# Kernel optimization log

Measured on AMD Instinct MI355X. Metric: run time of the kernel, lower is better.

The kernel has to match this reference:

```python
import jax, jax.numpy as jnp
import numpy as np

B, L, D, T, NL = 64, 512, 512, 5000, 2


def setup_inputs() -> dict:
    key = jax.random.key(0)
    k1, k2, k3, k4 = jax.random.split(key, 4)
    enc_output = jax.random.normal(k1, (B, L, D), dtype=jnp.float32)
    # stands in for the row/col-normalized tag co-occurrence matrix (values in [0, 0.01])
    ui_adj = jax.random.uniform(k2, (T, T), dtype=jnp.float32) * 0.01
    # one GCN weight matrix per layer in the layer_stack
    Ws = jax.random.normal(k3, (NL, D, D), dtype=jnp.float32) / np.sqrt(D).astype(np.float32)
    # event ids are 1-indexed in the original (it indexes with e - 1)
    event_type = jax.random.randint(k4, (B, L), 1, T + 1, dtype=jnp.int64)
    slf_attn_mask = jnp.zeros((B, L, L), dtype=bool)
    non_pad_mask = jnp.ones((B, L), dtype=bool)
    return {"enc_output": enc_output, "ui_adj": ui_adj, "Ws": Ws,
            "event_type": event_type, "slf_attn_mask": slf_attn_mask,
            "non_pad_mask": non_pad_mask}


def reference(enc_output, ui_adj, Ws, event_type, slf_attn_mask, non_pad_mask):
    # --- batched per-sample adjacency gather (replaces the Python loop) ---
    idx = event_type - 1                                   # [B, L] 0-indexed
    sub = ui_adj[idx[:, :, None], idx[:, None, :]]         # [B, L, L] = ui_adj[e-1,:][:, e-1]
    diag = ui_adj[idx, idx]                                # [B, L]   = ui_adj[e-1, e-1]
    adj = sub + diag[:, None, :]                           # vector broadcasts across rows, as in torch
    # --- GNN layer stack (hGCN layer ~ relu(A @ X @ W)) ---
    x = enc_output
    for l in range(Ws.shape[0]):                           # small fixed n_layers loop
        x = jax.nn.relu(jnp.einsum('bij,bjd->bid', adj, x) @ Ws[l])
    # --- mean pool over sequence ---
    return x.mean(axis=1)                                  # [B, D]
```

## Files before the change

kernel.cpp:

```cpp
#include <hip/hip_runtime.h>

typedef unsigned short u16;
typedef unsigned int u32;
typedef __bf16 bf16x8 __attribute__((ext_vector_type(8)));
typedef float f32x16 __attribute__((ext_vector_type(16)));
typedef int i32x4 __attribute__((ext_vector_type(4)));
typedef u32 u32x2 __attribute__((ext_vector_type(2)));
typedef u32 u32x4 __attribute__((ext_vector_type(4)));

#define T_ 5000
#define CAP 96

__device__ __forceinline__ u16 f2bf(float f) {
  u32 u = __float_as_uint(f);
  u += 0x7fffu + ((u >> 16) & 1u);
  return (u16)(u >> 16);
}
__device__ __forceinline__ float bf2f(u32 bits16) {
  return __uint_as_float(bits16 << 16);
}

__device__ __forceinline__ void gload_lds16(const u16* g, u16* l) {
  __builtin_amdgcn_global_load_lds(
      (__attribute__((address_space(1))) void*)(u16*)g,
      (__attribute__((address_space(3))) void*)l, 16, 0, 0);
}

__device__ __forceinline__ u32 lds_off(const void* p) {
  return (u32)(uintptr_t)(__attribute__((address_space(3))) const void*)p;
}

__device__ __forceinline__ u32 swz(int row, int kb) {
  return (u32)((row >> 1) * 128 +
               ((((row & 1) << 6) | kb) ^ (((row >> 1) & 7) << 4)));
}

__global__ void prep_k(const float* __restrict__ src, u16* __restrict__ dst,
                       int* __restrict__ cnt) {
  __shared__ float tile[32][33];
  const int tx = threadIdx.x, ty = threadIdx.y;
  const int a0 = blockIdx.x * 32;
  const int b0 = blockIdx.y * 32;
  const size_t zoff = (size_t)blockIdx.z * (512 * 512);
  const float* s = src + zoff;
  u16* d = dst + zoff;
#pragma unroll
  for (int r = 0; r < 4; ++r)
    tile[ty + r * 8][tx] = s[(size_t)(a0 + ty + r * 8) * 512 + b0 + tx];
  const int gid = ((blockIdx.z * 16 + blockIdx.y) * 16 + blockIdx.x) * 256 + ty * 32 + tx;
  if (gid < 5008) cnt[gid] = 0;
  __syncthreads();
#pragma unroll
  for (int r = 0; r < 4; ++r)
    d[(size_t)(b0 + ty + r * 8) * 512 + a0 + tx] = f2bf(tile[tx][ty + r * 8]);
}

__global__ void fill_k(const int* __restrict__ ev, const float* __restrict__ ui,
                       int2* __restrict__ cd, int* __restrict__ cnt,
                       int* __restrict__ list, int* __restrict__ ovf) {
  const int t = blockIdx.x * 256 + threadIdx.x;
  const int r = ev[t] - 1;
  int2 v;
  v.x = r;
  v.y = __float_as_int(ui[(size_t)r * (T_ + 1)]);
  cd[t] = v;
  const int pos = atomicAdd(&cnt[r], 1);
  if (pos < CAP) list[r * CAP + pos] = t;
  else { const int o = atomicAdd(&cnt[5000], 1); ovf[o] = t; }
}

__global__ __launch_bounds__(256)
void grow_gather(const float* __restrict__ ui, const int2* __restrict__ cd,
                 const int* __restrict__ cnt, const int* __restrict__ list,
                 const int* __restrict__ ovf, u16* __restrict__ adj) {
  __shared__ float row[5000];
  __shared__ int lst[CAP];
  const int r = blockIdx.x;
  int c = cnt[r];
  if (c > CAP) c = CAP;
  const int j = threadIdx.x * 2;
  if (c > 0) {
    const float* __restrict__ src = ui + (size_t)r * T_;
    for (int t = threadIdx.x; t < 1250; t += 256)
      *(float4*)&row[t * 4] = *(const float4*)&src[t * 4];
    if (threadIdx.x < c) lst[threadIdx.x] = list[r * CAP + threadIdx.x];
    __syncthreads();
    int q = 0;
    for (; q + 4 <= c; q += 4) {
      const int t0 = lst[q], t1 = lst[q + 1], t2 = lst[q + 2], t3 = lst[q + 3];
      const int4 p0 = *(const int4*)&cd[((t0 >> 9) << 9) + j];
      const int4 p1 = *(const int4*)&cd[((t1 >> 9) << 9) + j];
      const int4 p2 = *(const int4*)&cd[((t2 >> 9) << 9) + j];
      const int4 p3 = *(const int4*)&cd[((t3 >> 9) << 9) + j];
      const u32 k0 = (u32)f2bf(row[p0.x] + __int_as_float(p0.y)) |
                     ((u32)f2bf(row[p0.z] + __int_as_float(p0.w)) << 16);
      const u32 k1 = (u32)f2bf(row[p1.x] + __int_as_float(p1.y)) |
                     ((u32)f2bf(row[p1.z] + __int_as_float(p1.w)) << 16);
      const u32 k2 = (u32)f2bf(row[p2.x] + __int_as_float(p2.y)) |
                     ((u32)f2bf(row[p2.z] + __int_as_float(p2.w)) << 16);
      const u32 k3 = (u32)f2bf(row[p3.x] + __int_as_float(p3.y)) |
                     ((u32)f2bf(row[p3.z] + __int_as_float(p3.w)) << 16);
      *(u32*)&adj[(size_t)t0 * 512 + j] = k0;
      *(u32*)&adj[(size_t)t1 * 512 + j] = k1;
      *(u32*)&adj[(size_t)t2 * 512 + j] = k2;
      *(u32*)&adj[(size_t)t3 * 512 + j] = k3;
    }
    for (; q < c; ++q) {
      const int t0 = lst[q];
      const int4 p0 = *(const int4*)&cd[((t0 >> 9) << 9) + j];
      const u32 k0 = (u32)f2bf(row[p0.x] + __int_as_float(p0.y)) |
                     ((u32)f2bf(row[p0.z] + __int_as_float(p0.w)) << 16);
      *(u32*)&adj[(size_t)t0 * 512 + j] = k0;
    }
  }
  if (r < 8) {
    const int n = cnt[5000];
    for (int q = r; q < n; q += 8) {
      const int t = ovf[q];
      const long rr = (long)cd[t].x;
      const float* __restrict__ rp = ui + rr * (long)T_;
      const int4 p = *(const int4*)&cd[((t >> 9) << 9) + j];
      const u32 pk = (u32)f2bf(rp[p.x] + __int_as_float(p.y)) |
                     ((u32)f2bf(rp[p.z] + __int_as_float(p.w)) << 16);
      *(u32*)&adj[(size_t)t * 512 + j] = pk;
    }
  }
}

template <int MODE, int BSRC>
__global__ __launch_bounds__(512, 2)
void gemm256(const u16* __restrict__ A, const void* __restrict__ Bv,
             u16* __restrict__ C, size_t strideA, size_t strideB, size_t strideC,
             float* __restrict__ P) {
  extern __shared__ u16 smem[];
  const int tid = threadIdx.x;
  const int lane = tid & 63;
  const int w = tid >> 6;
  const int wm = w >> 2, wn = w & 3;
  const int chunk = gridDim.x >> 3;
  const int wg = blockIdx.x;
  const int mapped = (wg & 7) * chunk + (wg >> 3);
  const int batch = mapped >> 2;
  const int tm = (mapped >> 1) & 1, tn = mapped & 1;
  const int m0 = tm << 8, n0 = tn << 8;
  const u16* __restrict__ Ab = A + (size_t)batch * strideA;

  const u16* gA[2];
  u32 ldA[2];
#pragma unroll
  for (int r = 0; r < 2; ++r) {
    const int c = r * 512 + tid;
    const int L = c * 16;
    const int pp = L >> 7;
    const int off = (L & 127) ^ ((pp & 7) << 4);
    const int m = pp * 2 + (off >> 6);
    const int kb = off & 63;
    gA[r] = Ab + (size_t)(m0 + m) * 512 + (kb >> 1);
    ldA[r] = (u32)((r * 512 + w * 64) * 8);
  }

  const u16* gB[2] = {nullptr, nullptr};
  u32 ldB[2] = {0, 0};
  if (BSRC == 0) {
    const u16* __restrict__ Bb = (const u16*)Bv + (size_t)batch * strideB;
#pragma unroll
    for (int r = 0; r < 2; ++r) {
      const int c = r * 512 + tid;
      const int L = c * 16;
      const int pp = L >> 7;
      const int off = (L & 127) ^ ((pp & 7) << 4);
      const int m = pp * 2 + (off >> 6);
      const int kb = off & 63;
      gB[r] = Bb + (size_t)(n0 + m) * 512 + (kb >> 1);
      ldB[r] = (u32)(32768 + (r * 512 + w * 64) * 8);
    }
  }

  const int dp = tid & 127;
  const int lq = tid >> 7;
  unsigned long long encB = 0;
  u32 boff0 = 0;
  u32x2 bs0[8], bs1[8];
  if (BSRC == 1) {
    encB = (unsigned long long)(uintptr_t)((const float*)Bv + (size_t)batch * strideB);
    boff0 = (u32)(((lq * 8) * 512 + n0 + dp * 2) * 4);
  }

#define BLOAD(t, S)                                                          \
  {                                                                          \
    const u32 ob = boff0 + (u32)(t) * 65536u;                                \
    _Pragma("unroll") for (int i = 0; i < 8; ++i)                            \
        asm volatile("global_load_dwordx2 %0, %1, %2"                        \
                     : "=v"(S[i])                                            \
                     : "v"(ob + (u32)i * 2048u), "s"(encB));                 \
  }

#define CONVERT_B(S)                                                         \
  {                                                                          \
    u32 wrd0[4], wrd1[4];                                                    \
    _Pragma("unroll") for (int jj = 0; jj < 4; ++jj) {                       \
      asm("v_cvt_pk_bf16_f32 %0, %1, %2"                                     \
          : "=v"(wrd0[jj]) : "v"(S[2 * jj].x), "v"(S[2 * jj + 1].x));        \
      asm("v_cvt_pk_bf16_f32 %0, %1, %2"                                     \
          : "=v"(wrd1[jj]) : "v"(S[2 * jj].y), "v"(S[2 * jj + 1].y));        \
    }                                                                        \
    const u32 by0 = (u32)dp * 128u + ((((u32)lq * 16u)) ^ (((u32)dp & 7u) << 4)); \
    const u32 by1 = (u32)dp * 128u + ((64u | ((u32)lq * 16u)) ^ (((u32)dp & 7u) << 4)); \
    u32x4 v0, v1;                                                            \
    v0.x = wrd0[0]; v0.y = wrd0[1]; v0.z = wrd0[2]; v0.w = wrd0[3];          \
    v1.x = wrd1[0]; v1.y = wrd1[1]; v1.z = wrd1[2]; v1.w = wrd1[3];          \
    *(u32x4*)((char*)smem + 65536 + by0) = v0;                               \
    *(u32x4*)((char*)smem + 65536 + by1) = v1;                               \
  }

  const int col = lane & 31;
  const int h16 = (lane >> 5) * 16;
  u32 aOff[4][2], bOff[2][2];
#pragma unroll
  for (int mf = 0; mf < 4; ++mf)
#pragma unroll
    for (int kk = 0; kk < 2; ++kk)
      aOff[mf][kk] = swz(wm * 128 + mf * 32 + col, kk * 32 + h16);
#pragma unroll
  for (int nf = 0; nf < 2; ++nf)
#pragma unroll
    for (int kk = 0; kk < 2; ++kk)
      bOff[nf][kk] = 65536u + swz(wn * 64 + nf * 32 + col, kk * 32 + h16);
  const u32 ldsBase = lds_off(smem);

  f32x16 acc[4][2] = {};

  auto stageA = [&](int t) {
    const u32 bo = (u32)(t & 3) * 8192;
#pragma unroll
    for (int r = 0; r < 2; ++r) gload_lds16(gA[r] + t * 32, smem + bo + ldA[r]);
  };
  auto stageB0 = [&](int t) {
    const u32 bo = (u32)(t & 3) * 8192;
#pragma unroll
    for (int r = 0; r < 2; ++r) gload_lds16(gB[r] + t * 32, smem + bo + ldB[r]);
  };

  if (BSRC == 0) {
    stageA(0); stageB0(0); stageA(1); stageB0(1); stageA(2); stageB0(2);
  } else {
    stageA(0); stageA(1); stageA(2);
    BLOAD(0, bs0); BLOAD(1, bs1);
  }

#pragma unroll
  for (int t = 0; t < 16; ++t) {
    if (BSRC == 0) {
      if (t <= 13)      asm volatile("s_waitcnt vmcnt(8)" ::: "memory");
      else if (t == 14) asm volatile("s_waitcnt vmcnt(4)" ::: "memory");
      else              asm volatile("s_waitcnt vmcnt(0)" ::: "memory");
      __builtin_amdgcn_sched_barrier(0);
      if (t + 3 < 16) { stageA(t + 3); stageB0(t + 3); }
      asm volatile("" ::: "memory");
      __builtin_amdgcn_s_barrier();
      asm volatile("" ::: "memory");
    } else {
      if (t == 0)              asm volatile("s_waitcnt vmcnt(8)" ::: "memory");
      else if (t <= 13)        asm volatile("s_waitcnt vmcnt(10)" ::: "memory");
      else if (t == 14)        asm volatile("s_waitcnt vmcnt(8)" ::: "memory");
      else                     asm volatile("s_waitcnt vmcnt(0)" ::: "memory");
      __builtin_amdgcn_sched_barrier(0);
      if (t & 1) { CONVERT_B(bs1); } else { CONVERT_B(bs0); }
      if (t + 3 < 16) stageA(t + 3);
      if (t + 2 < 16) { if (t & 1) { BLOAD(t + 2, bs1); } else { BLOAD(t + 2, bs0); } }
      asm volatile("s_waitcnt lgkmcnt(0)" ::: "memory");
      __builtin_amdgcn_s_barrier();
      asm volatile("" ::: "memory");
    }

    const u32 abase = ldsBase + (u32)(t & 3) * 16384;
    const u32 bbase = (BSRC == 0) ? abase : ldsBase;
    i32x4 braw[2][2], araw[4][2];
#pragma unroll
    for (int nf = 0; nf < 2; ++nf)
#pragma unroll
      for (int kk = 0; kk < 2; ++kk)
        asm volatile("ds_read_b128 %0, %1" : "=v"(braw[nf][kk]) : "v"(bbase + bOff[nf][kk]));
#pragma unroll
    for (int mf = 0; mf < 2; ++mf)
#pragma unroll
      for (int kk = 0; kk < 2; ++kk)
        asm volatile("ds_read_b128 %0, %1" : "=v"(araw[mf][kk]) : "v"(abase + aOff[mf][kk]));
#pragma unroll
    for (int mf = 2; mf < 4; ++mf)
#pragma unroll
      for (int kk = 0; kk < 2; ++kk)
        asm volatile("ds_read_b128 %0, %1" : "=v"(araw[mf][kk]) : "v"(abase + aOff[mf][kk]));

    asm volatile("s_waitcnt lgkmcnt(4)" ::: "memory");
    __builtin_amdgcn_sched_barrier(0);
    __builtin_amdgcn_s_setprio(1);
#pragma unroll
    for (int kk = 0; kk < 2; ++kk)
#pragma unroll
      for (int mf = 0; mf < 2; ++mf)
#pragma unroll
        for (int nf = 0; nf < 2; ++nf)
          acc[mf][nf] = __builtin_amdgcn_mfma_f32_32x32x16_bf16(
              __builtin_bit_cast(bf16x8, araw[mf][kk]),
              __builtin_bit_cast(bf16x8, braw[nf][kk]), acc[mf][nf], 0, 0, 0);
    asm volatile("s_waitcnt lgkmcnt(0)" ::: "memory");
    __builtin_amdgcn_sched_barrier(0);
#pragma unroll
    for (int kk = 0; kk < 2; ++kk)
#pragma unroll
      for (int mf = 2; mf < 4; ++mf)
#pragma unroll
        for (int nf = 0; nf < 2; ++nf)
          acc[mf][nf] = __builtin_amdgcn_mfma_f32_32x32x16_bf16(
              __builtin_bit_cast(bf16x8, araw[mf][kk]),
              __builtin_bit_cast(bf16x8, braw[nf][kk]), acc[mf][nf], 0, 0, 0);
    __builtin_amdgcn_s_setprio(0);
    asm volatile("" ::: "memory");
    __builtin_amdgcn_s_barrier();
    __builtin_amdgcn_sched_barrier(0);
  }
#undef BLOAD
#undef CONVERT_B

  u16* Cb = C + (size_t)batch * strideC;
  if (MODE == 0) {
#pragma unroll
    for (int mf = 0; mf < 4; ++mf) {
      const int rbase = m0 + wm * 128 + mf * 32 + 4 * (lane >> 5);
#pragma unroll
      for (int nf = 0; nf < 2; ++nf) {
        const int cc = n0 + wn * 64 + nf * 32 + col;
        const f32x16 v = acc[mf][nf];
#pragma unroll
        for (int g = 0; g < 4; ++g)
#pragma unroll
          for (int j = 0; j < 4; ++j)
            Cb[(size_t)(rbase + 8 * g + j) * 512 + cc] = f2bf(v[g * 4 + j]);
      }
    }
  } else if (MODE == 1) {
#pragma unroll
    for (int mf = 0; mf < 4; ++mf) {
      const int ibase = m0 + wm * 128 + mf * 32 + 4 * (lane >> 5);
#pragma unroll
      for (int nf = 0; nf < 2; ++nf) {
        const int d = n0 + wn * 64 + nf * 32 + col;
        const f32x16 v = acc[mf][nf];
#pragma unroll
        for (int g = 0; g < 4; ++g) {
          const int i = ibase + 8 * g;
          uint2 p;
          p.x = (u32)f2bf(fmaxf(v[g * 4 + 0], 0.f)) |
                ((u32)f2bf(fmaxf(v[g * 4 + 1], 0.f)) << 16);
          p.y = (u32)f2bf(fmaxf(v[g * 4 + 2], 0.f)) |
                ((u32)f2bf(fmaxf(v[g * 4 + 3], 0.f)) << 16);
          *(uint2*)&Cb[(size_t)d * 512 + i] = p;
        }
      }
    }
  } else {
    const int slot = tm * 2 + wm;
#pragma unroll
    for (int nf = 0; nf < 2; ++nf) {
      float s = 0.f;
#pragma unroll
      for (int mf = 0; mf < 4; ++mf) {
        const f32x16 v = acc[mf][nf];
#pragma unroll
        for (int r = 0; r < 16; ++r) s += fmaxf(v[r], 0.f);
      }
      s += __shfl_xor(s, 32);
      if (lane < 32) {
        const int d = n0 + wn * 64 + nf * 32 + lane;
        P[((size_t)batch * 4 + slot) * 512 + d] = s;
      }
    }
  }
}

__global__ void reduce_mean(const float* __restrict__ P, float* __restrict__ out) {
  const int t = blockIdx.x * 256 + threadIdx.x;
  const int b = t >> 9, d = t & 511;
  float s = 0.f;
#pragma unroll
  for (int q = 0; q < 4; ++q) s += P[((size_t)b * 4 + q) * 512 + d];
  out[t] = s * (1.0f / 512.0f);
}

extern "C" void kernel_launch(void* const* d_in, const int* in_sizes, int n_in,
                              void* d_out, int out_size, void* d_ws, size_t ws_size,
                              hipStream_t stream) {
  const float* enc = (const float*)d_in[0];
  const float* ui  = (const float*)d_in[1];
  const float* Ws  = (const float*)d_in[2];
  const int*   ev  = (const int*)d_in[3];
  float* out = (float*)d_out;

  char* ws = (char*)d_ws;
  const size_t SLAB = (size_t)64 * 512 * 512 * 2;
  u16* adj  = (u16*)(ws);
  u16* tbuf = (u16*)(ws + SLAB);
  u16* xb   = (u16*)(ws + 2 * SLAB);
  char* p = ws + 3 * SLAB;
  u16* wst  = (u16*)p;  p += (size_t)2 * 512 * 512 * 2;
  int2* cd  = (int2*)p; p += (size_t)32768 * 8;
  int* cnt  = (int*)p;  p += 5008 * 4;
  int* list = (int*)p;  p += (size_t)5000 * CAP * 4;
  int* ovf  = (int*)p;  p += (size_t)32768 * 4;
  float* P  = (float*)p;

  const size_t PS = (size_t)512 * 512;
  const size_t SMEM0 = 131072;
  const size_t SMEM1 = 81920;
  (void)hipFuncSetAttribute(reinterpret_cast<const void*>(gemm256<0, 1>),
                            hipFuncAttributeMaxDynamicSharedMemorySize, (int)SMEM1);
  (void)hipFuncSetAttribute(reinterpret_cast<const void*>(gemm256<1, 0>),
                            hipFuncAttributeMaxDynamicSharedMemorySize, (int)SMEM0);
  (void)hipFuncSetAttribute(reinterpret_cast<const void*>(gemm256<0, 0>),
                            hipFuncAttributeMaxDynamicSharedMemorySize, (int)SMEM0);
  (void)hipFuncSetAttribute(reinterpret_cast<const void*>(gemm256<2, 0>),
                            hipFuncAttributeMaxDynamicSharedMemorySize, (int)SMEM0);

  prep_k<<<dim3(16, 16, 2), dim3(32, 8), 0, stream>>>(Ws, wst, cnt);
  fill_k<<<128, 256, 0, stream>>>(ev, ui, cd, cnt, list, ovf);
  grow_gather<<<5000, 256, 0, stream>>>(ui, cd, cnt, list, ovf, adj);
  gemm256<0, 1><<<256, 512, SMEM1, stream>>>(adj, enc, tbuf, PS, PS, PS, nullptr);
  gemm256<1, 0><<<256, 512, SMEM0, stream>>>(tbuf, wst, xb, PS, 0, PS, nullptr);
  gemm256<0, 0><<<256, 512, SMEM0, stream>>>(adj, xb, tbuf, PS, PS, PS, nullptr);
  gemm256<2, 0><<<256, 512, SMEM0, stream>>>(tbuf, wst + PS, nullptr, PS, 0, 0, P);
  reduce_mean<<<128, 256, 0, stream>>>(P, out);
}
```

Before: 144.9 us.

## Split GEMMs into 256x128 tiles with triple-buffered LDS and higher occupancy

```diff
diff --git a/kernel.cpp b/kernel.cpp
--- a/kernel.cpp
+++ b/kernel.cpp
@@ -6,7 +6,6 @@
 typedef float f32x16 __attribute__((ext_vector_type(16)));
 typedef int i32x4 __attribute__((ext_vector_type(4)));
 typedef u32 u32x2 __attribute__((ext_vector_type(2)));
-typedef u32 u32x4 __attribute__((ext_vector_type(4)));
 
 #define T_ 5000
 #define CAP 96
@@ -15,9 +14,6 @@
   u32 u = __float_as_uint(f);
   u += 0x7fffu + ((u >> 16) & 1u);
   return (u16)(u >> 16);
-}
-__device__ __forceinline__ float bf2f(u32 bits16) {
-  return __uint_as_float(bits16 << 16);
 }
 
 __device__ __forceinline__ void gload_lds16(const u16* g, u16* l) {
@@ -127,66 +123,62 @@
   }
 }
 
-template <int MODE, int BSRC>
-__global__ __launch_bounds__(512, 2)
-void gemm256(const u16* __restrict__ A, const void* __restrict__ Bv,
-             u16* __restrict__ C, size_t strideA, size_t strideB, size_t strideC,
-             float* __restrict__ P) {
+template <int LAYER>
+__global__ __launch_bounds__(512, LAYER == 0 ? 2 : 4)
+void gemmT(const u16* __restrict__ adj, const void* __restrict__ Xv,
+           u16* __restrict__ tb) {
   extern __shared__ u16 smem[];
   const int tid = threadIdx.x;
   const int lane = tid & 63;
   const int w = tid >> 6;
-  const int wm = w >> 2, wn = w & 3;
-  const int chunk = gridDim.x >> 3;
+  const int wm = w >> 1;
+  const int wn = w & 1;
   const int wg = blockIdx.x;
-  const int mapped = (wg & 7) * chunk + (wg >> 3);
-  const int batch = mapped >> 2;
-  const int tm = (mapped >> 1) & 1, tn = mapped & 1;
-  const int m0 = tm << 8, n0 = tn << 8;
-  const u16* __restrict__ Ab = A + (size_t)batch * strideA;
-
-  const u16* gA[2];
-  u32 ldA[2];
-#pragma unroll
-  for (int r = 0; r < 2; ++r) {
-    const int c = r * 512 + tid;
-    const int L = c * 16;
-    const int pp = L >> 7;
-    const int off = (L & 127) ^ ((pp & 7) << 4);
-    const int m = pp * 2 + (off >> 6);
+  const int mapped = (wg & 7) * 64 + (wg >> 3);
+  const int batch = mapped >> 3;
+  const int sub = mapped & 7;
+  const int m0 = (sub >> 2) << 8;
+  const int n0i = (sub & 3) << 7;
+  const size_t PS = (size_t)512 * 512;
+  const u16* __restrict__ adjB = adj + batch * PS;
+
+  const u16* gAdj;
+  u32 ldAdj;
+  {
+    const int L = tid * 16;
+    const int p = L >> 7;
+    const int off = (L & 127) ^ ((p & 7) << 4);
+    const int mr = p * 2 + (off >> 6);
     const int kb = off & 63;
-    gA[r] = Ab + (size_t)(m0 + m) * 512 + (kb >> 1);
-    ldA[r] = (u32)((r * 512 + w * 64) * 8);
-  }
-
-  const u16* gB[2] = {nullptr, nullptr};
-  u32 ldB[2] = {0, 0};
-  if (BSRC == 0) {
-    const u16* __restrict__ Bb = (const u16*)Bv + (size_t)batch * strideB;
+    gAdj = adjB + (size_t)(n0i + mr) * 512 + (kb >> 1);
+    ldAdj = (u32)(w * 512);
+  }
+  const u16* gX[2] = {nullptr, nullptr};
+  u32 ldX[2] = {0, 0};
+  unsigned long long encB = 0;
+  u32 boff0 = 0;
+  const int dp = tid & 127;
+  const int lq = tid >> 7;
+  u32x2 bs0[8], bs1[8];
+  if (LAYER == 1) {
+    const u16* __restrict__ xbB = (const u16*)Xv + batch * PS;
 #pragma unroll
     for (int r = 0; r < 2; ++r) {
       const int c = r * 512 + tid;
       const int L = c * 16;
-      const int pp = L >> 7;
-      const int off = (L & 127) ^ ((pp & 7) << 4);
-      const int m = pp * 2 + (off >> 6);
+      const int p = L >> 7;
+      const int off = (L & 127) ^ ((p & 7) << 4);
+      const int mr = p * 2 + (off >> 6);
       const int kb = off & 63;
-      gB[r] = Bb + (size_t)(n0 + m) * 512 + (kb >> 1);
-      ldB[r] = (u32)(32768 + (r * 512 + w * 64) * 8);
-    }
-  }
-
-  const int dp = tid & 127;
-  const int lq = tid >> 7;
-  unsigned long long encB = 0;
-  u32 boff0 = 0;
-  u32x2 bs0[8], bs1[8];
-  if (BSRC == 1) {
-    encB = (unsigned long long)(uintptr_t)((const float*)Bv + (size_t)batch * strideB);
-    boff0 = (u32)(((lq * 8) * 512 + n0 + dp * 2) * 4);
-  }
-
-#define BLOAD(t, S)                                                          \
+      gX[r] = xbB + (size_t)(m0 + mr) * 512 + (kb >> 1);
+      ldX[r] = (u32)(r * 4096 + w * 512);
+    }
+  } else {
+    encB = (unsigned long long)(uintptr_t)((const float*)Xv + batch * PS);
+    boff0 = (u32)(((lq * 8) * 512 + m0 + dp * 2) * 4);
+  }
+
+#define ELOAD(t, S)                                                          \
   {                                                                          \
     const u32 ob = boff0 + (u32)(t) * 65536u;                                \
     _Pragma("unroll") for (int i = 0; i < 8; ++i)                            \
@@ -195,7 +187,7 @@
                      : "v"(ob + (u32)i * 2048u), "s"(encB));                 \
   }
 
-#define CONVERT_B(S)                                                         \
+#define ECONV(S)                                                             \
   {                                                                          \
     u32 wrd0[4], wrd1[4];                                                    \
     _Pragma("unroll") for (int jj = 0; jj < 4; ++jj) {                       \
@@ -206,174 +198,270 @@
     }                                                                        \
     const u32 by0 = (u32)dp * 128u + ((((u32)lq * 16u)) ^ (((u32)dp & 7u) << 4)); \
     const u32 by1 = (u32)dp * 128u + ((64u | ((u32)lq * 16u)) ^ (((u32)dp & 7u) << 4)); \
-    u32x4 v0, v1;                                                            \
-    v0.x = wrd0[0]; v0.y = wrd0[1]; v0.z = wrd0[2]; v0.w = wrd0[3];          \
-    v1.x = wrd1[0]; v1.y = wrd1[1]; v1.z = wrd1[2]; v1.w = wrd1[3];          \
-    *(u32x4*)((char*)smem + 65536 + by0) = v0;                               \
-    *(u32x4*)((char*)smem + 65536 + by1) = v1;                               \
+    i32x4 v0, v1;                                                            \
+    v0.x = (int)wrd0[0]; v0.y = (int)wrd0[1]; v0.z = (int)wrd0[2]; v0.w = (int)wrd0[3]; \
+    v1.x = (int)wrd1[0]; v1.y = (int)wrd1[1]; v1.z = (int)wrd1[2]; v1.w = (int)wrd1[3]; \
+    *(i32x4*)((char*)smem + by0) = v0;                                       \
+    *(i32x4*)((char*)smem + by1) = v1;                                       \
   }
 
   const int col = lane & 31;
   const int h16 = (lane >> 5) * 16;
-  u32 aOff[4][2], bOff[2][2];
-#pragma unroll
-  for (int mf = 0; mf < 4; ++mf)
+  u32 xOff[2][2], adjOff[2][2];
+#pragma unroll
+  for (int df = 0; df < 2; ++df)
 #pragma unroll
     for (int kk = 0; kk < 2; ++kk)
-      aOff[mf][kk] = swz(wm * 128 + mf * 32 + col, kk * 32 + h16);
-#pragma unroll
-  for (int nf = 0; nf < 2; ++nf)
+      xOff[df][kk] = swz(wm * 64 + df * 32 + col, kk * 32 + h16);
+#pragma unroll
+  for (int f = 0; f < 2; ++f)
 #pragma unroll
     for (int kk = 0; kk < 2; ++kk)
-      bOff[nf][kk] = 65536u + swz(wn * 64 + nf * 32 + col, kk * 32 + h16);
+      adjOff[f][kk] = swz(wn * 64 + f * 32 + col, kk * 32 + h16);
   const u32 ldsBase = lds_off(smem);
-
-  f32x16 acc[4][2] = {};
-
-  auto stageA = [&](int t) {
-    const u32 bo = (u32)(t & 3) * 8192;
-#pragma unroll
-    for (int r = 0; r < 2; ++r) gload_lds16(gA[r] + t * 32, smem + bo + ldA[r]);
+  const u32 XBQ[3] = {LAYER == 0 ? 0u : 0u, LAYER == 0 ? 0u : 16384u,
+                      LAYER == 0 ? 0u : 32768u};
+  const u32 ABQ[3] = {LAYER == 0 ? 16384u : 49152u, LAYER == 0 ? 24576u : 57344u,
+                      LAYER == 0 ? 32768u : 65536u};
+
+  f32x16 acc[2][2] = {};
+
+  auto stageAdj = [&](int t) {
+    gload_lds16(gAdj + t * 32, smem + (ABQ[t % 3] >> 1) + ldAdj);
   };
-  auto stageB0 = [&](int t) {
-    const u32 bo = (u32)(t & 3) * 8192;
-#pragma unroll
-    for (int r = 0; r < 2; ++r) gload_lds16(gB[r] + t * 32, smem + bo + ldB[r]);
+  auto stageX = [&](int t) {
+#pragma unroll
+    for (int r = 0; r < 2; ++r)
+      gload_lds16(gX[r] + t * 32, smem + (XBQ[t % 3] >> 1) + ldX[r]);
   };
 
-  if (BSRC == 0) {
-    stageA(0); stageB0(0); stageA(1); stageB0(1); stageA(2); stageB0(2);
+  if (LAYER == 0) {
+    ELOAD(0, bs0); stageAdj(0); ELOAD(1, bs1); stageAdj(1);
   } else {
-    stageA(0); stageA(1); stageA(2);
-    BLOAD(0, bs0); BLOAD(1, bs1);
+    stageX(0); stageAdj(0); stageX(1); stageAdj(1);
   }
 
 #pragma unroll
   for (int t = 0; t < 16; ++t) {
-    if (BSRC == 0) {
-      if (t <= 13)      asm volatile("s_waitcnt vmcnt(8)" ::: "memory");
-      else if (t == 14) asm volatile("s_waitcnt vmcnt(4)" ::: "memory");
-      else              asm volatile("s_waitcnt vmcnt(0)" ::: "memory");
+    if (LAYER == 0) {
+      if (t <= 14) asm volatile("s_waitcnt vmcnt(9)" ::: "memory");
+      else         asm volatile("s_waitcnt vmcnt(0)" ::: "memory");
       __builtin_amdgcn_sched_barrier(0);
-      if (t + 3 < 16) { stageA(t + 3); stageB0(t + 3); }
-      asm volatile("" ::: "memory");
-      __builtin_amdgcn_s_barrier();
-      asm volatile("" ::: "memory");
+      if (t & 1) { ECONV(bs1); } else { ECONV(bs0); }
+      if (t + 2 < 16) { if (t & 1) { ELOAD(t + 2, bs1); } else { ELOAD(t + 2, bs0); } }
+      asm volatile("s_waitcnt lgkmcnt(0)" ::: "memory");
     } else {
-      if (t == 0)              asm volatile("s_waitcnt vmcnt(8)" ::: "memory");
-      else if (t <= 13)        asm volatile("s_waitcnt vmcnt(10)" ::: "memory");
-      else if (t == 14)        asm volatile("s_waitcnt vmcnt(8)" ::: "memory");
-      else                     asm volatile("s_waitcnt vmcnt(0)" ::: "memory");
+      if (t <= 14) asm volatile("s_waitcnt vmcnt(3)" ::: "memory");
+      else         asm volatile("s_waitcnt vmcnt(0)" ::: "memory");
       __builtin_amdgcn_sched_barrier(0);
-      if (t & 1) { CONVERT_B(bs1); } else { CONVERT_B(bs0); }
-      if (t + 3 < 16) stageA(t + 3);
-      if (t + 2 < 16) { if (t & 1) { BLOAD(t + 2, bs1); } else { BLOAD(t + 2, bs0); } }
-      asm volatile("s_waitcnt lgkmcnt(0)" ::: "memory");
-      __builtin_amdgcn_s_barrier();
-      asm volatile("" ::: "memory");
-    }
-
-    const u32 abase = ldsBase + (u32)(t & 3) * 16384;
-    const u32 bbase = (BSRC == 0) ? abase : ldsBase;
-    i32x4 braw[2][2], araw[4][2];
-#pragma unroll
-    for (int nf = 0; nf < 2; ++nf)
+    }
+    __builtin_amdgcn_s_barrier();
+    asm volatile("" ::: "memory");
+
+    const u32 xb_ = ldsBase + XBQ[t % 3];
+    const u32 ab_ = ldsBase + ABQ[t % 3];
+    i32x4 xr[2][2], ar[2][2];
+#pragma unroll
+    for (int df = 0; df < 2; ++df)
 #pragma unroll
       for (int kk = 0; kk < 2; ++kk)
-        asm volatile("ds_read_b128 %0, %1" : "=v"(braw[nf][kk]) : "v"(bbase + bOff[nf][kk]));
-#pragma unroll
-    for (int mf = 0; mf < 2; ++mf)
+        asm volatile("ds_read_b128 %0, %1" : "=v"(xr[df][kk]) : "v"(xb_ + xOff[df][kk]));
+#pragma unroll
+    for (int f = 0; f < 2; ++f)
 #pragma unroll
       for (int kk = 0; kk < 2; ++kk)
-        asm volatile("ds_read_b128 %0, %1" : "=v"(araw[mf][kk]) : "v"(abase + aOff[mf][kk]));
-#pragma unroll
-    for (int mf = 2; mf < 4; ++mf)
-#pragma unroll
-      for (int kk = 0; kk < 2; ++kk)
-        asm volatile("ds_read_b128 %0, %1" : "=v"(araw[mf][kk]) : "v"(abase + aOff[mf][kk]));
-
-    asm volatile("s_waitcnt lgkmcnt(4)" ::: "memory");
-    __builtin_amdgcn_sched_barrier(0);
-    __builtin_amdgcn_s_setprio(1);
-#pragma unroll
-    for (int kk = 0; kk < 2; ++kk)
-#pragma unroll
-      for (int mf = 0; mf < 2; ++mf)
-#pragma unroll
-        for (int nf = 0; nf < 2; ++nf)
-          acc[mf][nf] = __builtin_amdgcn_mfma_f32_32x32x16_bf16(
-              __builtin_bit_cast(bf16x8, araw[mf][kk]),
-              __builtin_bit_cast(bf16x8, braw[nf][kk]), acc[mf][nf], 0, 0, 0);
+        asm volatile("ds_read_b128 %0, %1" : "=v"(ar[f][kk]) : "v"(ab_ + adjOff[f][kk]));
     asm volatile("s_waitcnt lgkmcnt(0)" ::: "memory");
     __builtin_amdgcn_sched_barrier(0);
+
+    __builtin_amdgcn_s_setprio(1);
 #pragma unroll
     for (int kk = 0; kk < 2; ++kk)
 #pragma unroll
-      for (int mf = 2; mf < 4; ++mf)
-#pragma unroll
-        for (int nf = 0; nf < 2; ++nf)
-          acc[mf][nf] = __builtin_amdgcn_mfma_f32_32x32x16_bf16(
-              __builtin_bit_cast(bf16x8, araw[mf][kk]),
-              __builtin_bit_cast(bf16x8, braw[nf][kk]), acc[mf][nf], 0, 0, 0);
+      for (int df = 0; df < 2; ++df)
+#pragma unroll
+        for (int f = 0; f < 2; ++f)
+          acc[df][f] = __builtin_amdgcn_mfma_f32_32x32x16_bf16(
+              __builtin_bit_cast(bf16x8, xr[df][kk]),
+              __builtin_bit_cast(bf16x8, ar[f][kk]), acc[df][f], 0, 0, 0);
     __builtin_amdgcn_s_setprio(0);
     asm volatile("" ::: "memory");
     __builtin_amdgcn_s_barrier();
     __builtin_amdgcn_sched_barrier(0);
-  }
-#undef BLOAD
-#undef CONVERT_B
-
-  u16* Cb = C + (size_t)batch * strideC;
-  if (MODE == 0) {
-#pragma unroll
-    for (int mf = 0; mf < 4; ++mf) {
-      const int rbase = m0 + wm * 128 + mf * 32 + 4 * (lane >> 5);
-#pragma unroll
-      for (int nf = 0; nf < 2; ++nf) {
-        const int cc = n0 + wn * 64 + nf * 32 + col;
-        const f32x16 v = acc[mf][nf];
-#pragma unroll
-        for (int g = 0; g < 4; ++g)
-#pragma unroll
-          for (int j = 0; j < 4; ++j)
-            Cb[(size_t)(rbase + 8 * g + j) * 512 + cc] = f2bf(v[g * 4 + j]);
+    if (t + 2 < 16) {
+      if (LAYER == 1) stageX(t + 2);
+      stageAdj(t + 2);
+    }
+  }
+#undef ELOAD
+#undef ECONV
+
+  u16* tbB = tb + batch * PS;
+#pragma unroll
+  for (int df = 0; df < 2; ++df)
+#pragma unroll
+    for (int f = 0; f < 2; ++f) {
+      const int i = n0i + wn * 64 + f * 32 + col;
+      const int dbase = m0 + wm * 64 + df * 32 + 4 * (lane >> 5);
+      const f32x16 v = acc[df][f];
+#pragma unroll
+      for (int g = 0; g < 4; ++g) {
+        uint2 p;
+        p.x = (u32)f2bf(v[g * 4 + 0]) | ((u32)f2bf(v[g * 4 + 1]) << 16);
+        p.y = (u32)f2bf(v[g * 4 + 2]) | ((u32)f2bf(v[g * 4 + 3]) << 16);
+        *(uint2*)&tbB[(size_t)i * 512 + dbase + 8 * g] = p;
       }
     }
-  } else if (MODE == 1) {
-#pragma unroll
-    for (int mf = 0; mf < 4; ++mf) {
-      const int ibase = m0 + wm * 128 + mf * 32 + 4 * (lane >> 5);
-#pragma unroll
-      for (int nf = 0; nf < 2; ++nf) {
-        const int d = n0 + wn * 64 + nf * 32 + col;
-        const f32x16 v = acc[mf][nf];
+}
+
+template <int MODE>
+__global__ __launch_bounds__(512, 4)
+void gemmW(const u16* __restrict__ tbuf, const u16* __restrict__ wstL,
+           u16* __restrict__ xbo, float* __restrict__ P) {
+  extern __shared__ u16 smem[];
+  const int tid = threadIdx.x;
+  const int lane = tid & 63;
+  const int w = tid >> 6;
+  const int wm = w >> 1;
+  const int wn = w & 1;
+  const int wg = blockIdx.x;
+  const int mapped = (wg & 7) * 64 + (wg >> 3);
+  const int batch = mapped >> 3;
+  const int sub = mapped & 7;
+  const int it = sub >> 2;
+  const int i0 = it << 8;
+  const int e0 = (sub & 3) << 7;
+  const size_t PS = (size_t)512 * 512;
+  const u16* __restrict__ Ab = tbuf + batch * PS;
+
+  const u16* gA[2];
+  u32 ldA[2];
+#pragma unroll
+  for (int r = 0; r < 2; ++r) {
+    const int c = r * 512 + tid;
+    const int L = c * 16;
+    const int p = L >> 7;
+    const int off = (L & 127) ^ ((p & 7) << 4);
+    const int mr = p * 2 + (off >> 6);
+    const int kb = off & 63;
+    gA[r] = Ab + (size_t)(i0 + mr) * 512 + (kb >> 1);
+    ldA[r] = (u32)(r * 4096 + w * 512);
+  }
+  const u16* gB;
+  u32 ldB;
+  {
+    const int L = tid * 16;
+    const int p = L >> 7;
+    const int off = (L & 127) ^ ((p & 7) << 4);
+    const int mr = p * 2 + (off >> 6);
+    const int kb = off & 63;
+    gB = wstL + (size_t)(e0 + mr) * 512 + (kb >> 1);
+    ldB = (u32)(w * 512);
+  }
+
+  const int col = lane & 31;
+  const int h16 = (lane >> 5) * 16;
+  u32 aOff[2][2], bOff[2][2];
+#pragma unroll
+  for (int mi = 0; mi < 2; ++mi)
+#pragma unroll
+    for (int kk = 0; kk < 2; ++kk)
+      aOff[mi][kk] = swz(wm * 64 + mi * 32 + col, kk * 32 + h16);
+#pragma unroll
+  for (int ne = 0; ne < 2; ++ne)
+#pragma unroll
+    for (int kk = 0; kk < 2; ++kk)
+      bOff[ne][kk] = swz(wn * 64 + ne * 32 + col, kk * 32 + h16);
+  const u32 ldsBase = lds_off(smem);
+  const u32 ABQ[3] = {0u, 16384u, 32768u};
+  const u32 BBQ[3] = {49152u, 57344u, 65536u};
+
+  f32x16 acc[2][2] = {};
+
+  auto stage = [&](int t) {
+#pragma unroll
+    for (int r = 0; r < 2; ++r)
+      gload_lds16(gA[r] + t * 32, smem + (ABQ[t % 3] >> 1) + ldA[r]);
+    gload_lds16(gB + t * 32, smem + (BBQ[t % 3] >> 1) + ldB);
+  };
+
+  stage(0); stage(1);
+
+#pragma unroll
+  for (int t = 0; t < 16; ++t) {
+    if (t <= 14) asm volatile("s_waitcnt vmcnt(3)" ::: "memory");
+    else         asm volatile("s_waitcnt vmcnt(0)" ::: "memory");
+    __builtin_amdgcn_sched_barrier(0);
+    __builtin_amdgcn_s_barrier();
+    asm volatile("" ::: "memory");
+
+    const u32 ab_ = ldsBase + ABQ[t % 3];
+    const u32 bb_ = ldsBase + BBQ[t % 3];
+    i32x4 ar[2][2], br[2][2];
+#pragma unroll
+    for (int mi = 0; mi < 2; ++mi)
+#pragma unroll
+      for (int kk = 0; kk < 2; ++kk)
+        asm volatile("ds_read_b128 %0, %1" : "=v"(ar[mi][kk]) : "v"(ab_ + aOff[mi][kk]));
+#pragma unroll
+    for (int ne = 0; ne < 2; ++ne)
+#pragma unroll
+      for (int kk = 0; kk < 2; ++kk)
+        asm volatile("ds_read_b128 %0, %1" : "=v"(br[ne][kk]) : "v"(bb_ + bOff[ne][kk]));
+    asm volatile("s_waitcnt lgkmcnt(0)" ::: "memory");
+    __builtin_amdgcn_sched_barrier(0);
+
+    __builtin_amdgcn_s_setprio(1);
+#pragma unroll
+    for (int kk = 0; kk < 2; ++kk)
+#pragma unroll
+      for (int mi = 0; mi < 2; ++mi)
+#pragma unroll
+        for (int ne = 0; ne < 2; ++ne)
+          acc[mi][ne] = __builtin_amdgcn_mfma_f32_32x32x16_bf16(
+              __builtin_bit_cast(bf16x8, ar[mi][kk]),
+              __builtin_bit_cast(bf16x8, br[ne][kk]), acc[mi][ne], 0, 0, 0);
+    __builtin_amdgcn_s_setprio(0);
+    asm volatile("" ::: "memory");
+    __builtin_amdgcn_s_barrier();
+    __builtin_amdgcn_sched_barrier(0);
+    if (t + 2 < 16) stage(t + 2);
+  }
+
+  if (MODE == 1) {
+    u16* xbB = xbo + batch * PS;
+#pragma unroll
+    for (int mi = 0; mi < 2; ++mi)
+#pragma unroll
+      for (int ne = 0; ne < 2; ++ne) {
+        const int e = e0 + wn * 64 + ne * 32 + col;
+        const int ibase = i0 + wm * 64 + mi * 32 + 4 * (lane >> 5);
+        const f32x16 v = acc[mi][ne];
 #pragma unroll
         for (int g = 0; g < 4; ++g) {
-          const int i = ibase + 8 * g;
           uint2 p;
           p.x = (u32)f2bf(fmaxf(v[g * 4 + 0], 0.f)) |
                 ((u32)f2bf(fmaxf(v[g * 4 + 1], 0.f)) << 16);
           p.y = (u32)f2bf(fmaxf(v[g * 4 + 2], 0.f)) |
                 ((u32)f2bf(fmaxf(v[g * 4 + 3], 0.f)) << 16);
-          *(uint2*)&Cb[(size_t)d * 512 + i] = p;
+          *(uint2*)&xbB[(size_t)e * 512 + ibase + 8 * g] = p;
         }
       }
-    }
   } else {
-    const int slot = tm * 2 + wm;
-#pragma unroll
-    for (int nf = 0; nf < 2; ++nf) {
+#pragma unroll
+    for (int ne = 0; ne < 2; ++ne) {
       float s = 0.f;
 #pragma unroll
-      for (int mf = 0; mf < 4; ++mf) {
-        const f32x16 v = acc[mf][nf];
+      for (int mi = 0; mi < 2; ++mi) {
+        const f32x16 v = acc[mi][ne];
 #pragma unroll
         for (int r = 0; r < 16; ++r) s += fmaxf(v[r], 0.f);
       }
       s += __shfl_xor(s, 32);
       if (lane < 32) {
-        const int d = n0 + wn * 64 + nf * 32 + lane;
-        P[((size_t)batch * 4 + slot) * 512 + d] = s;
+        const int e = e0 + wn * 64 + ne * 32 + lane;
+        const int slot = it * 4 + wm;
+        P[((size_t)batch * 8 + slot) * 512 + e] = s;
       }
     }
   }
@@ -384,7 +472,7 @@
   const int b = t >> 9, d = t & 511;
   float s = 0.f;
 #pragma unroll
-  for (int q = 0; q < 4; ++q) s += P[((size_t)b * 4 + q) * 512 + d];
+  for (int q = 0; q < 8; ++q) s += P[((size_t)b * 8 + q) * 512 + d];
   out[t] = s * (1.0f / 512.0f);
 }
 
@@ -411,23 +499,24 @@
   float* P  = (float*)p;
 
   const size_t PS = (size_t)512 * 512;
-  const size_t SMEM0 = 131072;
-  const size_t SMEM1 = 81920;
-  (void)hipFuncSetAttribute(reinterpret_cast<const void*>(gemm256<0, 1>),
-                            hipFuncAttributeMaxDynamicSharedMemorySize, (int)SMEM1);
-  (void)hipFuncSetAttribute(reinterpret_cast<const void*>(gemm256<1, 0>),
-                            hipFuncAttributeMaxDynamicSharedMemorySize, (int)SMEM0);
-  (void)hipFuncSetAttribute(reinterpret_cast<const void*>(gemm256<0, 0>),
-                            hipFuncAttributeMaxDynamicSharedMemorySize, (int)SMEM0);
-  (void)hipFuncSetAttribute(reinterpret_cast<const void*>(gemm256<2, 0>),
-                            hipFuncAttributeMaxDynamicSharedMemorySize, (int)SMEM0);
+  const size_t SM_T0 = 40960;
+  const size_t SM_T1 = 73728;
+  const size_t SM_W  = 73728;
+  (void)hipFuncSetAttribute(reinterpret_cast<const void*>(gemmT<0>),
+                            hipFuncAttributeMaxDynamicSharedMemorySize, (int)SM_T0);
+  (void)hipFuncSetAttribute(reinterpret_cast<const void*>(gemmT<1>),
+                            hipFuncAttributeMaxDynamicSharedMemorySize, (int)SM_T1);
+  (void)hipFuncSetAttribute(reinterpret_cast<const void*>(gemmW<1>),
+                            hipFuncAttributeMaxDynamicSharedMemorySize, (int)SM_W);
+  (void)hipFuncSetAttribute(reinterpret_cast<const void*>(gemmW<2>),
+                            hipFuncAttributeMaxDynamicSharedMemorySize, (int)SM_W);
 
   prep_k<<<dim3(16, 16, 2), dim3(32, 8), 0, stream>>>(Ws, wst, cnt);
   fill_k<<<128, 256, 0, stream>>>(ev, ui, cd, cnt, list, ovf);
   grow_gather<<<5000, 256, 0, stream>>>(ui, cd, cnt, list, ovf, adj);
-  gemm256<0, 1><<<256, 512, SMEM1, stream>>>(adj, enc, tbuf, PS, PS, PS, nullptr);
-  gemm256<1, 0><<<256, 512, SMEM0, stream>>>(tbuf, wst, xb, PS, 0, PS, nullptr);
-  gemm256<0, 0><<<256, 512, SMEM0, stream>>>(adj, xb, tbuf, PS, PS, PS, nullptr);
-  gemm256<2, 0><<<256, 512, SMEM0, stream>>>(tbuf, wst + PS, nullptr, PS, 0, 0, P);
+  gemmT<0><<<512, 512, SM_T0, stream>>>(adj, enc, tbuf);
+  gemmW<1><<<512, 512, SM_W, stream>>>(tbuf, wst, xb, nullptr);
+  gemmT<1><<<512, 512, SM_T1, stream>>>(adj, xb, tbuf);
+  gemmW<2><<<512, 512, SM_W, stream>>>(tbuf, wst + PS, nullptr, P);
   reduce_mean<<<128, 256, 0, stream>>>(P, out);
 }
```

Result: slower. 172.8 us (+19.2%).
